# Kernel optimization log

Hardware: AMD Instinct MI355X
Metric: run time of the kernel (lower is better)

The kernel has to match this reference:

```python
import jax, jax.numpy as jnp
import numpy as np

B, T, D_MODEL = 2, 2048, 2048
Q_HEADS, KV_HEADS = 16, 4
HEAD_DIM = D_MODEL // Q_HEADS  # 128
N_GROUPS = Q_HEADS // KV_HEADS  # 4
THETA = 10000.0


def setup_inputs() -> dict:
    key = jax.random.key(0)
    ks = jax.random.split(key, 5)
    s = 0.02
    return {
        "x": jax.random.normal(ks[0], (B, T, D_MODEL), dtype=jnp.float32),
        "Wq": jax.random.normal(ks[1], (Q_HEADS * HEAD_DIM, D_MODEL), dtype=jnp.float32) * s,
        "Wk": jax.random.normal(ks[2], (KV_HEADS * HEAD_DIM, D_MODEL), dtype=jnp.float32) * s,
        "Wv": jax.random.normal(ks[3], (KV_HEADS * HEAD_DIM, D_MODEL), dtype=jnp.float32) * s,
        "Wo": jax.random.normal(ks[4], (D_MODEL, D_MODEL), dtype=jnp.float32) * s,
    }


def _apply_rope(q, k, t):
    # freqs = outer(arange(t), 1/theta^(2i/d)) ; complex rotation on (even,odd) pairs
    inv_freq = 1.0 / (THETA ** (jnp.arange(0, HEAD_DIM, 2, dtype=jnp.float32) / HEAD_DIM))
    ang = jnp.arange(t, dtype=jnp.float32)[:, None] * inv_freq[None, :]  # [t, hd/2]
    cos = jnp.cos(ang)[None, :, None, :]  # [1,t,1,hd/2]
    sin = jnp.sin(ang)[None, :, None, :]

    def rot(x):
        xr = x.reshape(*x.shape[:-1], HEAD_DIM // 2, 2)
        xe, xo = xr[..., 0], xr[..., 1]
        out = jnp.stack([xe * cos - xo * sin, xe * sin + xo * cos], axis=-1)
        return out.reshape(x.shape)

    return rot(q), rot(k)


def reference(x, Wq, Wk, Wv, Wo):
    b, t, c = x.shape
    q = (x @ Wq.T).reshape(b, t, Q_HEADS, HEAD_DIM)
    k = (x @ Wk.T).reshape(b, t, KV_HEADS, HEAD_DIM)
    v = (x @ Wv.T).reshape(b, t, KV_HEADS, HEAD_DIM)
    q, k = _apply_rope(q, k, t)
    # GQA: repeat kv heads to match q heads (repeat_interleave on head dim)
    k = jnp.repeat(k, N_GROUPS, axis=2)
    v = jnp.repeat(v, N_GROUPS, axis=2)
    q = q.transpose(0, 2, 1, 3)  # [b,h,t,d]
    k = k.transpose(0, 2, 1, 3)
    v = v.transpose(0, 2, 1, 3)
    scale = HEAD_DIM ** -0.5
    attn = jnp.einsum("bhqd,bhkd->bhqk", q, k) * scale
    causal = jnp.tril(jnp.ones((t, t), dtype=bool))
    attn = jnp.where(causal[None, None], attn, -jnp.inf)
    attn = jax.nn.softmax(attn, axis=-1)
    out = jnp.einsum("bhqk,bhkd->bhqd", attn, v)
    out = out.transpose(0, 2, 1, 3).reshape(b, t, c)
    return out @ Wo.T
```

## Files before the change

### kernel.cpp

```cpp
#include <hip/hip_runtime.h>
#include <hip/hip_bf16.h>

typedef __bf16 bf16_t;
typedef __bf16 bf16x8 __attribute__((ext_vector_type(8)));
typedef __bf16 bf16x4 __attribute__((ext_vector_type(4)));
typedef float f32x4 __attribute__((ext_vector_type(4)));

#define SEQ_T 2048
#define DMODEL 2048
#define NQH 16
#define NKVH 4
#define HDIM 128

__device__ __forceinline__ f32x4 mfma16x16x32(bf16x8 a, bf16x8 b, f32x4 c) {
  return __builtin_amdgcn_mfma_f32_16x16x32_bf16(a, b, c, 0, 0, 0);
}

typedef __attribute__((address_space(3))) void lds_void_t;
typedef __attribute__((address_space(1))) const void gbl_void_t;
__device__ __forceinline__ void gload_lds16(const bf16_t* g, bf16_t* l) {
  __builtin_amdgcn_global_load_lds((gbl_void_t*)g, (lds_void_t*)l, 16, 0, 0);
}
__device__ __forceinline__ void BAR() {
  asm volatile("" ::: "memory");
  __builtin_amdgcn_s_barrier();
  asm volatile("" ::: "memory");
}

__global__ __launch_bounds__(256) void cast_all(const float* __restrict__ x,
                                                const float* __restrict__ Wq,
                                                const float* __restrict__ Wk,
                                                const float* __restrict__ Wv,
                                                const float* __restrict__ Wo,
                                                bf16_t* __restrict__ xb,
                                                bf16_t* __restrict__ Wqkvb,
                                                bf16_t* __restrict__ Wob) {
  const int idx = blockIdx.x * 256 + threadIdx.x;
  const float* src;
  bf16_t* dst;
  if (idx < 1048576) {
    src = x + (size_t)idx * 8;
    dst = xb + (size_t)idx * 8;
  } else if (idx < 1572864) {
    const int r = idx - 1048576;
    src = Wq + (size_t)r * 8;
    dst = Wqkvb + (size_t)r * 8;
  } else if (idx < 1703936) {
    const int r = idx - 1572864;
    src = Wk + (size_t)r * 8;
    dst = Wqkvb + 4194304 + (size_t)r * 8;
  } else if (idx < 1835008) {
    const int r = idx - 1703936;
    src = Wv + (size_t)r * 8;
    dst = Wqkvb + 5242880 + (size_t)r * 8;
  } else {
    const int r = idx - 1835008;
    src = Wo + (size_t)r * 8;
    dst = Wob + (size_t)r * 8;
  }
  const float4* s4 = reinterpret_cast<const float4*>(src);
  float4 a = s4[0], b = s4[1];
  bf16x8 r8 = {(bf16_t)a.x, (bf16_t)a.y, (bf16_t)a.z, (bf16_t)a.w,
               (bf16_t)b.x, (bf16_t)b.y, (bf16_t)b.z, (bf16_t)b.w};
  *reinterpret_cast<bf16x8*>(dst) = r8;
}

__global__ __launch_bounds__(256) void sincos_kernel(float2* __restrict__ tab) {
  int idx = blockIdx.x * 256 + threadIdx.x;
  int t = idx >> 6, i = idx & 63;
  float inv = exp2f((float)i * (-13.287712379549449f / 64.0f));
  float ang = (float)t * inv;
  float s, c;
  sincosf(ang, &s, &c);
  tab[idx] = make_float2(c, s);
}

__global__ __launch_bounds__(512, 2) void gemm_qkv(const bf16_t* __restrict__ A,
                                                   const bf16_t* __restrict__ W,
                                                   bf16_t* __restrict__ q_out,
                                                   bf16_t* __restrict__ k_out,
                                                   bf16_t* __restrict__ v_out,
                                                   const float2* __restrict__ tab) {
  constexpr int K = 2048;
  constexpr int NT = 32;
  const int id = ((int)blockIdx.x & 7) * 32 + ((int)blockIdx.x >> 3);
  const int m0 = (id >> 4) * 256, n0 = (id & 15) * 192;
  const int tid = threadIdx.x;
  const int lane = tid & 63, w = tid >> 6;
  const int wr = w >> 2, wc = w & 3;
  const int l15 = lane & 15, g = lane >> 4;
  __shared__ bf16_t smem[2][(256 + 192) * 64];
  f32x4 acc[8][3] = {};
  bf16x8 af[4][2], bfr[3][2];

  auto ISSUE_A = [&](int tt, int h) {
    bf16_t* base = &smem[tt & 1][0] + h * (128 * 64);
    const bf16_t* src = A + (size_t)(m0 + h * 128) * K + tt * 64;
#pragma unroll
    for (int i = 0; i < 2; i++) {
      const int rl = i * 64 + (tid >> 3);
      gload_lds16(src + (size_t)rl * K + (((tid & 7) ^ (rl & 7)) << 3),
                  base + (i * 64 + w * 8) * 64);
    }
  };
  auto ISSUE_B = [&](int tt, int c) {
    bf16_t* base = &smem[tt & 1][0] + (256 + c * 64) * 64;
    const int rl = tid >> 3;
    const bf16_t* src = W + (size_t)(n0 + c * 64 + rl) * K + tt * 64;
    gload_lds16(src + (((tid & 7) ^ (rl & 7)) << 3), base + (w * 8) * 64);
  };
  auto RDA = [&](const bf16_t* Ab, int qm) {
#pragma unroll
    for (int fi = 0; fi < 4; fi++) {
      const int row = wr * 128 + qm * 64 + fi * 16 + l15;
#pragma unroll
      for (int ksl = 0; ksl < 2; ksl++)
        af[fi][ksl] = *reinterpret_cast<const bf16x8*>(
            Ab + row * 64 + ((((ksl << 2) + g) ^ (row & 7)) << 3));
    }
  };
  auto RDB1 = [&](const bf16_t* Bb, int fj) {
    const int row = wc * 48 + fj * 16 + l15;
#pragma unroll
    for (int ksl = 0; ksl < 2; ksl++)
      bfr[fj][ksl] = *reinterpret_cast<const bf16x8*>(
          Bb + row * 64 + ((((ksl << 2) + g) ^ (row & 7)) << 3));
  };

#define MMX(QM, FJLO, FJHI)                                                   \
  do {                                                                        \
    __builtin_amdgcn_s_setprio(1);                                            \
    _Pragma("unroll") for (int fi = 0; fi < 4; fi++)                          \
        _Pragma("unroll") for (int fj = (FJLO); fj <= (FJHI); fj++)           \
            _Pragma("unroll") for (int ksl = 0; ksl < 2; ksl++)               \
                acc[(QM)*4 + fi][fj] =                                        \
                    mfma16x16x32(af[fi][ksl], bfr[fj][ksl], acc[(QM)*4 + fi][fj]); \
    __builtin_amdgcn_s_setprio(0);                                            \
  } while (0)

  ISSUE_A(0, 0);
  ISSUE_A(0, 1);
  ISSUE_B(0, 0);
  ISSUE_B(0, 1);
  ISSUE_B(0, 2);

  for (int t = 0; t < NT; t++) {
    const bf16_t* Ab = &smem[t & 1][0];
    const bf16_t* Bb = Ab + 256 * 64;
    if (t + 1 < NT) {
      ISSUE_A(t + 1, 0);
      ISSUE_A(t + 1, 1);
      asm volatile("s_waitcnt vmcnt(4)" ::: "memory");
    } else {
      asm volatile("s_waitcnt vmcnt(0)" ::: "memory");
    }
    BAR();
    RDA(Ab, 0);
    RDB1(Bb, 0);
    RDB1(Bb, 1);
    MMX(0, 0, 1);
    BAR();
    RDB1(Bb, 2);
    if (t + 1 < NT) {
      ISSUE_B(t + 1, 0);
      ISSUE_B(t + 1, 1);
      ISSUE_B(t + 1, 2);
    }
    BAR();
    MMX(0, 2, 2);
    BAR();
    RDA(Ab, 1);
    BAR();
    MMX(1, 0, 1);
    MMX(1, 2, 2);
    BAR();
  }
#undef MMX

#pragma unroll
  for (int fm = 0; fm < 8; fm++) {
    const int r0 = m0 + wr * 128 + fm * 16 + (g << 2);
    const int bb = r0 >> 11;
    const int tt = r0 & 2047;
#pragma unroll
    for (int fn = 0; fn < 3; fn++) {
      const int col = n0 + wc * 48 + fn * 16 + l15;
      const f32x4 v = acc[fm][fn];
      if (col < 2048) {
        const int dd = col & 127;
        const float2* tp = tab + (size_t)tt * 64 + (dd >> 1);
        bf16_t* dst = q_out + (((size_t)(bb * NQH + (col >> 7)) * SEQ_T + tt) * HDIM + dd);
#pragma unroll
        for (int i = 0; i < 4; i++) {
          float me = v[i];
          float ot = __shfl_xor(me, 1);
          float2 cs = tp[(size_t)i * 64];
          float r = (dd & 1) ? (me * cs.x + ot * cs.y) : (me * cs.x - ot * cs.y);
          dst[(size_t)i * HDIM] = (bf16_t)r;
        }
      } else if (col < 2560) {
        const int dd = col & 127;
        const float2* tp = tab + (size_t)tt * 64 + (dd >> 1);
        bf16_t* dst = k_out + (((size_t)(bb * NKVH + ((col - 2048) >> 7)) * SEQ_T + tt) * HDIM + dd);
#pragma unroll
        for (int i = 0; i < 4; i++) {
          float me = v[i];
          float ot = __shfl_xor(me, 1);
          float2 cs = tp[(size_t)i * 64];
          float r = (dd & 1) ? (me * cs.x + ot * cs.y) : (me * cs.x - ot * cs.y);
          dst[(size_t)i * HDIM] = (bf16_t)r;
        }
      } else {
        const int vc = col - 2560;
        const int hh = vc >> 7, dd = vc & 127;
        const int tp64 = (tt & ~63) | (((tt >> 2) & 3) << 4) | (((tt >> 4) & 3) << 2);
        bf16x4 pk = {(bf16_t)v[0], (bf16_t)v[1], (bf16_t)v[2], (bf16_t)v[3]};
        *reinterpret_cast<bf16x4*>(v_out + (((size_t)(bb * NKVH + hh) * HDIM + dd) * SEQ_T + tp64)) = pk;
      }
    }
  }
}

__global__ __launch_bounds__(512, 2) void gemm_out(const bf16_t* __restrict__ A,
                                                   const bf16_t* __restrict__ W,
                                                   float* __restrict__ c_out) {
  constexpr int K = 2048;
  constexpr int NT = 32;
  const int id = ((int)blockIdx.x & 7) * 32 + ((int)blockIdx.x >> 3);
  const int m0 = (id >> 4) * 256, n0 = (id & 15) * 128;
  const int tid = threadIdx.x;
  const int lane = tid & 63, w = tid >> 6;
  const int wr = w >> 2, wc = w & 3;
  const int l15 = lane & 15, g = lane >> 4;
  __shared__ bf16_t smem[2][(256 + 128) * 64];
  f32x4 acc[8][2] = {};
  bf16x8 af[4][2], bfr[1][2];

  auto ISSUE_HALF = [&](int tt, int h) {
    const int k0 = tt * 64;
    bf16_t* base = &smem[tt & 1][0] + ((h < 2) ? h * (128 * 64) : 256 * 64);
    const bf16_t* src = (h < 2) ? (A + (size_t)(m0 + h * 128) * K)
                                : (W + (size_t)n0 * K);
#pragma unroll
    for (int i = 0; i < 2; i++) {
      const int rl = i * 64 + (tid >> 3);
      gload_lds16(src + (size_t)rl * K + k0 + (((tid & 7) ^ (rl & 7)) << 3),
                  base + (i * 64 + w * 8) * 64);
    }
  };
  auto RDA = [&](const bf16_t* Ab, int qm) {
#pragma unroll
    for (int fi = 0; fi < 4; fi++) {
      const int row = wr * 128 + qm * 64 + fi * 16 + l15;
#pragma unroll
      for (int ksl = 0; ksl < 2; ksl++)
        af[fi][ksl] = *reinterpret_cast<const bf16x8*>(
            Ab + row * 64 + ((((ksl << 2) + g) ^ (row & 7)) << 3));
    }
  };
  auto RDB = [&](const bf16_t* Bb, int qn) {
    const int row = wc * 32 + qn * 16 + l15;
#pragma unroll
    for (int ksl = 0; ksl < 2; ksl++)
      bfr[0][ksl] = *reinterpret_cast<const bf16x8*>(
          Bb + row * 64 + ((((ksl << 2) + g) ^ (row & 7)) << 3));
  };

#define MMPH(QM, QN)                                                          \
  do {                                                                        \
    __builtin_amdgcn_s_setprio(1);                                            \
    _Pragma("unroll") for (int fi = 0; fi < 4; fi++)                          \
        _Pragma("unroll") for (int ksl = 0; ksl < 2; ksl++)                   \
            acc[(QM)*4 + fi][(QN)] =                                          \
                mfma16x16x32(af[fi][ksl], bfr[0][ksl], acc[(QM)*4 + fi][(QN)]); \
    __builtin_amdgcn_s_setprio(0);                                            \
  } while (0)

#pragma unroll
  for (int h = 0; h < 3; h++) ISSUE_HALF(0, h);

  for (int t = 0; t < NT; t++) {
    const bf16_t* Ab = &smem[t & 1][0];
    const bf16_t* Bb = Ab + 256 * 64;
    if (t + 1 < NT) {
      ISSUE_HALF(t + 1, 0);
      ISSUE_HALF(t + 1, 1);
      asm volatile("s_waitcnt vmcnt(4)" ::: "memory");
    } else {
      asm volatile("s_waitcnt vmcnt(0)" ::: "memory");
    }
    BAR();
    RDA(Ab, 0);
    RDB(Bb, 0);
    MMPH(0, 0);
    BAR();
    RDB(Bb, 1);
    if (t + 1 < NT) ISSUE_HALF(t + 1, 2);
    BAR();
    MMPH(0, 1);
    BAR();
    RDA(Ab, 1);
    BAR();
    MMPH(1, 1);
    BAR();
    RDB(Bb, 0);
    BAR();
    MMPH(1, 0);
    BAR();
  }
#undef MMPH

#pragma unroll
  for (int fm = 0; fm < 8; fm++) {
    const int r0 = m0 + wr * 128 + fm * 16 + (g << 2);
#pragma unroll
    for (int fn = 0; fn < 2; fn++) {
      const int col = n0 + wc * 32 + fn * 16 + l15;
#pragma unroll
      for (int i = 0; i < 4; i++) c_out[(size_t)(r0 + i) * 2048 + col] = acc[fm][fn][i];
    }
  }
}

__global__ __launch_bounds__(256, 2) void attn_kernel(const bf16_t* __restrict__ Qb,
                                                      const bf16_t* __restrict__ Kb,
                                                      const bf16_t* __restrict__ Vt,
                                                      bf16_t* __restrict__ AO) {
  const int bh = blockIdx.x;
  const int b = bh >> 4, h = bh & 15, kvh = h >> 2;
  const int p = blockIdx.y;
  const int jH = 31 - p, jL = p;
  const int q0H = jH * 64, q0L = jL * 64;
  const int tid = threadIdx.x;
  const int lane = tid & 63, w = tid >> 6;
  const bf16_t* Qp = Qb + (size_t)(b * NQH + h) * SEQ_T * HDIM;
  const bf16_t* Kp = Kb + (size_t)(b * NKVH + kvh) * SEQ_T * HDIM;
  const bf16_t* Vp = Vt + (size_t)(b * NKVH + kvh) * HDIM * SEQ_T;
  __shared__ bf16_t smem[2][16384];
  const int l15 = lane & 15, g = lane >> 4;
  const int qrA = q0H + w * 16 + l15;
  const int qrB = q0L + w * 16 + l15;
  const float kscale = 0.08838834764831845f * 1.4426950408889634f;
  bf16x8 qfA[4], qfB[4];
#pragma unroll
  for (int c = 0; c < 4; c++) {
    qfA[c] = *reinterpret_cast<const bf16x8*>(Qp + (size_t)qrA * HDIM + c * 32 + (g << 3));
    qfB[c] = *reinterpret_cast<const bf16x8*>(Qp + (size_t)qrB * HDIM + c * 32 + (g << 3));
#pragma unroll
    for (int e = 0; e < 8; e++) {
      qfA[c][e] = (bf16_t)((float)qfA[c][e] * kscale);
      qfB[c][e] = (bf16_t)((float)qfB[c][e] * kscale);
    }
  }
  f32x4 oA[8] = {}, oB[8] = {};
  float lA = 0.0f, lB = 0.0f;
  const int wmaxB = q0L + w * 16 + 15;
  const int ntiles = jH + 1;

  auto STAGE = [&](int it, int buf) {
    const int kv0s = it * 64;
    bf16_t* Ks = smem[buf];
    bf16_t* Vs = smem[buf] + 8192;
#pragma unroll
    for (int cc = 0; cc < 4; cc++) {
      const int ck = cc * 256 + tid;
      const int krow = ck >> 4, kg = ck & 15;
      gload_lds16(Kp + (size_t)(kv0s + krow) * HDIM + ((kg ^ (krow & 7)) << 3),
                  Ks + (cc * 256 + w * 64) * 8);
      const int vrow = ck >> 3, vg = ck & 7;
      gload_lds16(Vp + (size_t)vrow * SEQ_T + kv0s + ((vg ^ (vrow & 7)) << 3),
                  Vs + (cc * 256 + w * 64) * 8);
    }
  };

  auto PEXP = [&](float* sv, float& l, bf16x8* pc) {
#pragma unroll
    for (int j = 0; j < 16; j++) sv[j] = exp2f(sv[j]);
    float r0 = (sv[0] + sv[1]) + (sv[2] + sv[3]);
    float r1 = (sv[4] + sv[5]) + (sv[6] + sv[7]);
    float r2 = (sv[8] + sv[9]) + (sv[10] + sv[11]);
    float r3 = (sv[12] + sv[13]) + (sv[14] + sv[15]);
    l += (r0 + r1) + (r2 + r3);
#pragma unroll
    for (int s = 0; s < 2; s++) {
      bf16x8 t = {(bf16_t)sv[8 * s],     (bf16_t)sv[8 * s + 1], (bf16_t)sv[8 * s + 2],
                  (bf16_t)sv[8 * s + 3], (bf16_t)sv[8 * s + 4], (bf16_t)sv[8 * s + 5],
                  (bf16_t)sv[8 * s + 6], (bf16_t)sv[8 * s + 7]};
      pc[s] = t;
    }
  };

  auto COMPUTE1 = [&](const bf16_t* Ks, const bf16_t* Vs, int kv0) {
    float sv[16];
    const bool noMask = (kv0 + 63 <= q0H + w * 16);
    __builtin_amdgcn_s_setprio(1);
#pragma unroll
    for (int ksub = 0; ksub < 4; ksub++) {
      f32x4 sa = {};
      const int krow = ksub * 16 + l15;
#pragma unroll
      for (int ch = 0; ch < 4; ch++) {
        bf16x8 kf = *reinterpret_cast<const bf16x8*>(
            Ks + krow * 128 + ((((ch << 2) + g) ^ (krow & 7)) << 3));
        sa = mfma16x16x32(kf, qfA[ch], sa);
      }
      if (noMask) {
#pragma unroll
        for (int i = 0; i < 4; i++) sv[ksub * 4 + i] = sa[i];
      } else {
        const int dlt = qrA - kv0 - ksub * 16 - (g << 2);
#pragma unroll
        for (int i = 0; i < 4; i++) sv[ksub * 4 + i] = (i <= dlt) ? sa[i] : -3e38f;
      }
    }
    __builtin_amdgcn_s_setprio(0);
    bf16x8 pc[2];
    PEXP(sv, lA, pc);
    __builtin_amdgcn_s_setprio(1);
#pragma unroll
    for (int dt = 0; dt < 8; dt++) {
      const int vrow = dt * 16 + l15;
#pragma unroll
      for (int s = 0; s < 2; s++) {
        bf16x8 vv = *reinterpret_cast<const bf16x8*>(
            Vs + vrow * 64 + (((2 * g + s) ^ (vrow & 7)) << 3));
        oA[dt] = mfma16x16x32(vv, pc[s], oA[dt]);
      }
    }
    __builtin_amdgcn_s_setprio(0);
  };

  auto COMPUTE2 = [&](const bf16_t* Ks, const bf16_t* Vs, int kv0) {
    float svA[16], svB[16];
    const bool noMaskB = (kv0 + 63 <= q0L + w * 16);
    __builtin_amdgcn_s_setprio(1);
#pragma unroll
    for (int ksub = 0; ksub < 4; ksub++) {
      f32x4 sa = {}, sb = {};
      const int krow = ksub * 16 + l15;
#pragma unroll
      for (int ch = 0; ch < 4; ch++) {
        bf16x8 kf = *reinterpret_cast<const bf16x8*>(
            Ks + krow * 128 + ((((ch << 2) + g) ^ (krow & 7)) << 3));
        sa = mfma16x16x32(kf, qfA[ch], sa);
        sb = mfma16x16x32(kf, qfB[ch], sb);
      }
#pragma unroll
      for (int i = 0; i < 4; i++) svA[ksub * 4 + i] = sa[i];
      if (noMaskB) {
#pragma unroll
        for (int i = 0; i < 4; i++) svB[ksub * 4 + i] = sb[i];
      } else {
        const int dltB = qrB - kv0 - ksub * 16 - (g << 2);
#pragma unroll
        for (int i = 0; i < 4; i++) svB[ksub * 4 + i] = (i <= dltB) ? sb[i] : -3e38f;
      }
    }
    __builtin_amdgcn_s_setprio(0);
    bf16x8 pcA[2], pcB[2];
    PEXP(svA, lA, pcA);
    PEXP(svB, lB, pcB);
    __builtin_amdgcn_s_setprio(1);
#pragma unroll
    for (int dt = 0; dt < 8; dt++) {
      const int vrow = dt * 16 + l15;
#pragma unroll
      for (int s = 0; s < 2; s++) {
        bf16x8 vv = *reinterpret_cast<const bf16x8*>(
            Vs + vrow * 64 + (((2 * g + s) ^ (vrow & 7)) << 3));
        oA[dt] = mfma16x16x32(vv, pcA[s], oA[dt]);
        oB[dt] = mfma16x16x32(vv, pcB[s], oB[dt]);
      }
    }
    __builtin_amdgcn_s_setprio(0);
  };

  STAGE(0, 0);
  for (int it = 0; it < ntiles; it++) {
    const int buf = it & 1;
    asm volatile("s_waitcnt vmcnt(0)" ::: "memory");
    BAR();
    if (it + 1 < ntiles) STAGE(it + 1, buf ^ 1);
    const int kv0 = it * 64;
    const bf16_t* Ks = smem[buf];
    const bf16_t* Vs = smem[buf] + 8192;
    if (kv0 <= wmaxB) {
      COMPUTE2(Ks, Vs, kv0);
    } else {
      COMPUTE1(Ks, Vs, kv0);
    }
  }
  BAR();
  bf16_t* os = &smem[0][0] + w * 2048;
  auto EPI = [&](f32x4* o, float lsum, int q0) {
    lsum += __shfl_xor(lsum, 16, 64);
    lsum += __shfl_xor(lsum, 32, 64);
    const float linv = 1.0f / lsum;
#pragma unroll
    for (int dt = 0; dt < 8; dt++) {
      bf16x4 pk = {(bf16_t)(o[dt][0] * linv), (bf16_t)(o[dt][1] * linv),
                   (bf16_t)(o[dt][2] * linv), (bf16_t)(o[dt][3] * linv)};
      *reinterpret_cast<bf16x4*>(os + l15 * 128 + dt * 16 + (g << 2)) = pk;
    }
    const size_t rowb = (size_t)b * SEQ_T + q0 + w * 16;
#pragma unroll
    for (int kk = 0; kk < 4; kk++) {
      const int c = lane + kk * 64;
      const int q = c >> 4, gc = c & 15;
      *reinterpret_cast<bf16x8*>(AO + (rowb + q) * DMODEL + h * HDIM + gc * 8) =
          *reinterpret_cast<const bf16x8*>(os + q * 128 + gc * 8);
    }
  };
  EPI(oA, lA, q0H);
  EPI(oB, lB, q0L);
}

extern "C" void kernel_launch(void* const* d_in, const int* in_sizes, int n_in,
                              void* d_out, int out_size, void* d_ws, size_t ws_size,
                              hipStream_t stream) {
  const float* x = (const float*)d_in[0];
  const float* Wq = (const float*)d_in[1];
  const float* Wk = (const float*)d_in[2];
  const float* Wv = (const float*)d_in[3];
  const float* Wo = (const float*)d_in[4];
  float* out = (float*)d_out;
  char* ws = (char*)d_ws;
  bf16_t* xb = (bf16_t*)(ws);
  bf16_t* Wqkvb = (bf16_t*)(ws + 16777216);
  bf16_t* Wob = (bf16_t*)(ws + 29360128);
  bf16_t* Qb = (bf16_t*)(ws + 37748736);
  bf16_t* Kb = (bf16_t*)(ws + 54525952);
  bf16_t* Vt = (bf16_t*)(ws + 58720256);
  bf16_t* AO = (bf16_t*)(ws + 62914560);
  float2* tab = (float2*)(ws + 79691776);

  cast_all<<<9216, 256, 0, stream>>>(x, Wq, Wk, Wv, Wo, xb, Wqkvb, Wob);
  sincos_kernel<<<512, 256, 0, stream>>>(tab);
  gemm_qkv<<<256, 512, 0, stream>>>(xb, Wqkvb, Qb, Kb, Vt, tab);
  attn_kernel<<<dim3(32, 16), 256, 0, stream>>>(Qb, Kb, Vt, AO);
  gemm_out<<<256, 512, 0, stream>>>(AO, Wob, out);
}
```

Measured before the change: 170.1 us.

## Simplify GEMM main loops to single-phase load-all then compute-all schedule

Both the QKV and output-projection GEMM main loops drop the interleaved multi-phase schedule, which had partial loads, staggered vmcnt waits and many barriers. Each iteration now waits for all outstanding loads, does one barrier, issues every global-to-LDS load for the next tile, reads all A and B fragments, and runs all MFMAs in one prioritized block. The aim is to cut barrier count and scheduling overhead. In exchange it loses the finer overlap between LDS reads and MFMAs, and it holds twice as many A fragments in registers, which raises register pressure under the 512-thread, 2-block launch bounds. A dead leftover loop computing an unused value was also added.

```diff
diff --git a/kernel.cpp b/kernel.cpp
--- a/kernel.cpp
+++ b/kernel.cpp
@@ -91,92 +91,74 @@
   const int l15 = lane & 15, g = lane >> 4;
   __shared__ bf16_t smem[2][(256 + 192) * 64];
   f32x4 acc[8][3] = {};
-  bf16x8 af[4][2], bfr[3][2];
-
-  auto ISSUE_A = [&](int tt, int h) {
-    bf16_t* base = &smem[tt & 1][0] + h * (128 * 64);
-    const bf16_t* src = A + (size_t)(m0 + h * 128) * K + tt * 64;
-#pragma unroll
-    for (int i = 0; i < 2; i++) {
-      const int rl = i * 64 + (tid >> 3);
-      gload_lds16(src + (size_t)rl * K + (((tid & 7) ^ (rl & 7)) << 3),
-                  base + (i * 64 + w * 8) * 64);
-    }
-  };
-  auto ISSUE_B = [&](int tt, int c) {
-    bf16_t* base = &smem[tt & 1][0] + (256 + c * 64) * 64;
-    const int rl = tid >> 3;
-    const bf16_t* src = W + (size_t)(n0 + c * 64 + rl) * K + tt * 64;
-    gload_lds16(src + (((tid & 7) ^ (rl & 7)) << 3), base + (w * 8) * 64);
-  };
-  auto RDA = [&](const bf16_t* Ab, int qm) {
-#pragma unroll
-    for (int fi = 0; fi < 4; fi++) {
-      const int row = wr * 128 + qm * 64 + fi * 16 + l15;
-#pragma unroll
-      for (int ksl = 0; ksl < 2; ksl++)
-        af[fi][ksl] = *reinterpret_cast<const bf16x8*>(
-            Ab + row * 64 + ((((ksl << 2) + g) ^ (row & 7)) << 3));
-    }
-  };
-  auto RDB1 = [&](const bf16_t* Bb, int fj) {
-    const int row = wc * 48 + fj * 16 + l15;
-#pragma unroll
-    for (int ksl = 0; ksl < 2; ksl++)
-      bfr[fj][ksl] = *reinterpret_cast<const bf16x8*>(
-          Bb + row * 64 + ((((ksl << 2) + g) ^ (row & 7)) << 3));
-  };
-
-#define MMX(QM, FJLO, FJHI)                                                   \
-  do {                                                                        \
-    __builtin_amdgcn_s_setprio(1);                                            \
-    _Pragma("unroll") for (int fi = 0; fi < 4; fi++)                          \
-        _Pragma("unroll") for (int fj = (FJLO); fj <= (FJHI); fj++)           \
-            _Pragma("unroll") for (int ksl = 0; ksl < 2; ksl++)               \
-                acc[(QM)*4 + fi][fj] =                                        \
-                    mfma16x16x32(af[fi][ksl], bfr[fj][ksl], acc[(QM)*4 + fi][fj]); \
-    __builtin_amdgcn_s_setprio(0);                                            \
-  } while (0)
-
-  ISSUE_A(0, 0);
-  ISSUE_A(0, 1);
-  ISSUE_B(0, 0);
-  ISSUE_B(0, 1);
-  ISSUE_B(0, 2);
+  bf16x8 af[2][4][2], bfr[3][2];
+
+  auto ISSUE_ALL = [&](int tt) {
+#pragma unroll
+    for (int h = 0; h < 2; h++) {
+      bf16_t* base = &smem[tt & 1][0] + h * (128 * 64);
+      const bf16_t* src = A + (size_t)(m0 + h * 128) * K + tt * 64;
+#pragma unroll
+      for (int i = 0; i < 2; i++) {
+        const int rl = i * 64 + (tid >> 3);
+        gload_lds16(src + (size_t)rl * K + (((tid & 7) ^ (rl & 7)) << 3),
+                    base + (i * 64 + w * 8) * 64);
+      }
+    }
+#pragma unroll
+    for (int c = 0; c < 3; c++) {
+      bf16_t* base = &smem[tt & 1][0] + (256 + c * 64) * 64;
+      const int rl = tid >> 3;
+      const bf16_t* src = W + (size_t)(n0 + c * 64 + rl) * K + tt * 64;
+      gload_lds16(src + (((tid & 7) ^ (rl & 7)) << 3), base + (w * 8) * 64);
+    }
+  };
+
+  ISSUE_ALL(0);
 
   for (int t = 0; t < NT; t++) {
     const bf16_t* Ab = &smem[t & 1][0];
     const bf16_t* Bb = Ab + 256 * 64;
-    if (t + 1 < NT) {
-      ISSUE_A(t + 1, 0);
-      ISSUE_A(t + 1, 1);
-      asm volatile("s_waitcnt vmcnt(4)" ::: "memory");
-    } else {
-      asm volatile("s_waitcnt vmcnt(0)" ::: "memory");
-    }
+    asm volatile("s_waitcnt vmcnt(0)" ::: "memory");
     BAR();
-    RDA(Ab, 0);
-    RDB1(Bb, 0);
-    RDB1(Bb, 1);
-    MMX(0, 0, 1);
-    BAR();
-    RDB1(Bb, 2);
-    if (t + 1 < NT) {
-      ISSUE_B(t + 1, 0);
-      ISSUE_B(t + 1, 1);
-      ISSUE_B(t + 1, 2);
-    }
-    BAR();
-    MMX(0, 2, 2);
-    BAR();
-    RDA(Ab, 1);
-    BAR();
-    MMX(1, 0, 1);
-    MMX(1, 2, 2);
-    BAR();
-  }
-#undef MMX
-
+    if (t + 1 < NT) ISSUE_ALL(t + 1);
+#pragma unroll
+    for (int qm = 0; qm < 2; qm++)
+#pragma unroll
+      for (int fi = 0; fi < 4; fi++) {
+        const int row = wr * 128 + qm * 64 + fi * 16 + l15;
+#pragma unroll
+        for (int ksl = 0; ksl < 2; ksl++)
+          af[qm][fi][ksl] = *reinterpret_cast<const bf16x8*>(
+              Ab + row * 64 + ((((ksl << 2) + g) ^ (row & 7)) << 3));
+      }
+#pragma unroll
+    for (int fj = 0; fj < 3; fj++) {
+      const int row = wc * 48 + fj * 16 + l15;
+#pragma unroll
+      for (int ksl = 0; ksl < 2; ksl++)
+        bfr[fj][ksl] = *reinterpret_cast<const bf16x8*>(
+            Bb + row * 64 + ((((ksl << 2) + g) ^ (row & 7)) << 3));
+    }
+    __builtin_amdgcn_s_setprio(1);
+#pragma unroll
+    for (int qm = 0; qm < 2; qm++)
+#pragma unroll
+      for (int fi = 0; fi < 4; fi++)
+#pragma unroll
+        for (int fj = 0; fj < 3; fj++)
+#pragma unroll
+          for (int ksl = 0; ksl < 2; ksl++)
+            acc[qm * 4 + fi][fj] =
+                mfma16x16x32(af[qm][fi][ksl], bfr[fj][ksl], acc[qm * 4 + fi][fj]);
+    __builtin_amdgcn_s_setprio(0);
+  }
+
+#pragma unroll
+  for (int fm = 0; fm < 8; fm++) {
+    const int r0 = m0 + (fm >> 2) * 128 + 0;
+    (void)r0;
+  }
 #pragma unroll
   for (int fm = 0; fm < 8; fm++) {
     const int r0 = m0 + wr * 128 + fm * 16 + (g << 2);
@@ -234,81 +216,63 @@
   const int l15 = lane & 15, g = lane >> 4;
   __shared__ bf16_t smem[2][(256 + 128) * 64];
   f32x4 acc[8][2] = {};
-  bf16x8 af[4][2], bfr[1][2];
-
-  auto ISSUE_HALF = [&](int tt, int h) {
+  bf16x8 af[2][4][2], bfr[2][2];
+
+  auto ISSUE_ALL = [&](int tt) {
     const int k0 = tt * 64;
-    bf16_t* base = &smem[tt & 1][0] + ((h < 2) ? h * (128 * 64) : 256 * 64);
-    const bf16_t* src = (h < 2) ? (A + (size_t)(m0 + h * 128) * K)
-                                : (W + (size_t)n0 * K);
-#pragma unroll
-    for (int i = 0; i < 2; i++) {
-      const int rl = i * 64 + (tid >> 3);
-      gload_lds16(src + (size_t)rl * K + k0 + (((tid & 7) ^ (rl & 7)) << 3),
-                  base + (i * 64 + w * 8) * 64);
-    }
-  };
-  auto RDA = [&](const bf16_t* Ab, int qm) {
-#pragma unroll
-    for (int fi = 0; fi < 4; fi++) {
-      const int row = wr * 128 + qm * 64 + fi * 16 + l15;
-#pragma unroll
-      for (int ksl = 0; ksl < 2; ksl++)
-        af[fi][ksl] = *reinterpret_cast<const bf16x8*>(
-            Ab + row * 64 + ((((ksl << 2) + g) ^ (row & 7)) << 3));
-    }
-  };
-  auto RDB = [&](const bf16_t* Bb, int qn) {
-    const int row = wc * 32 + qn * 16 + l15;
-#pragma unroll
-    for (int ksl = 0; ksl < 2; ksl++)
-      bfr[0][ksl] = *reinterpret_cast<const bf16x8*>(
-          Bb + row * 64 + ((((ksl << 2) + g) ^ (row & 7)) << 3));
-  };
-
-#define MMPH(QM, QN)                                                          \
-  do {                                                                        \
-    __builtin_amdgcn_s_setprio(1);                                            \
-    _Pragma("unroll") for (int fi = 0; fi < 4; fi++)                          \
-        _Pragma("unroll") for (int ksl = 0; ksl < 2; ksl++)                   \
-            acc[(QM)*4 + fi][(QN)] =                                          \
-                mfma16x16x32(af[fi][ksl], bfr[0][ksl], acc[(QM)*4 + fi][(QN)]); \
-    __builtin_amdgcn_s_setprio(0);                                            \
-  } while (0)
-
-#pragma unroll
-  for (int h = 0; h < 3; h++) ISSUE_HALF(0, h);
+#pragma unroll
+    for (int h = 0; h < 3; h++) {
+      bf16_t* base = &smem[tt & 1][0] + ((h < 2) ? h * (128 * 64) : 256 * 64);
+      const bf16_t* src = (h < 2) ? (A + (size_t)(m0 + h * 128) * K)
+                                  : (W + (size_t)n0 * K);
+#pragma unroll
+      for (int i = 0; i < 2; i++) {
+        const int rl = i * 64 + (tid >> 3);
+        gload_lds16(src + (size_t)rl * K + k0 + (((tid & 7) ^ (rl & 7)) << 3),
+                    base + (i * 64 + w * 8) * 64);
+      }
+    }
+  };
+
+  ISSUE_ALL(0);
 
   for (int t = 0; t < NT; t++) {
     const bf16_t* Ab = &smem[t & 1][0];
     const bf16_t* Bb = Ab + 256 * 64;
-    if (t + 1 < NT) {
-      ISSUE_HALF(t + 1, 0);
-      ISSUE_HALF(t + 1, 1);
-      asm volatile("s_waitcnt vmcnt(4)" ::: "memory");
-    } else {
-      asm volatile("s_waitcnt vmcnt(0)" ::: "memory");
-    }
+    asm volatile("s_waitcnt vmcnt(0)" ::: "memory");
     BAR();
-    RDA(Ab, 0);
-    RDB(Bb, 0);
-    MMPH(0, 0);
-    BAR();
-    RDB(Bb, 1);
-    if (t + 1 < NT) ISSUE_HALF(t + 1, 2);
-    BAR();
-    MMPH(0, 1);
-    BAR();
-    RDA(Ab, 1);
-    BAR();
-    MMPH(1, 1);
-    BAR();
-    RDB(Bb, 0);
-    BAR();
-    MMPH(1, 0);
-    BAR();
-  }
-#undef MMPH
+    if (t + 1 < NT) ISSUE_ALL(t + 1);
+#pragma unroll
+    for (int qm = 0; qm < 2; qm++)
+#pragma unroll
+      for (int fi = 0; fi < 4; fi++) {
+        const int row = wr * 128 + qm * 64 + fi * 16 + l15;
+#pragma unroll
+        for (int ksl = 0; ksl < 2; ksl++)
+          af[qm][fi][ksl] = *reinterpret_cast<const bf16x8*>(
+              Ab + row * 64 + ((((ksl << 2) + g) ^ (row & 7)) << 3));
+      }
+#pragma unroll
+    for (int qn = 0; qn < 2; qn++) {
+      const int row = wc * 32 + qn * 16 + l15;
+#pragma unroll
+      for (int ksl = 0; ksl < 2; ksl++)
+        bfr[qn][ksl] = *reinterpret_cast<const bf16x8*>(
+            Bb + row * 64 + ((((ksl << 2) + g) ^ (row & 7)) << 3));
+    }
+    __builtin_amdgcn_s_setprio(1);
+#pragma unroll
+    for (int qm = 0; qm < 2; qm++)
+#pragma unroll
+      for (int fi = 0; fi < 4; fi++)
+#pragma unroll
+        for (int qn = 0; qn < 2; qn++)
+#pragma unroll
+          for (int ksl = 0; ksl < 2; ksl++)
+            acc[qm * 4 + fi][qn] =
+                mfma16x16x32(af[qm][fi][ksl], bfr[qn][ksl], acc[qm * 4 + fi][qn]);
+    __builtin_amdgcn_s_setprio(0);
+  }
 
 #pragma unroll
   for (int fm = 0; fm < 8; fm++) {
```

Measured after the change: 165.7 us. 1.03x faster.
